# Performance work log

Hardware: AMD Instinct MI355X
Metric: run time of the kernel (lower is better)

Reference implementation:

```python
import jax, jax.numpy as jnp
import numpy as np

TOP_K = 2  # num_experts_per_tok


def setup_inputs() -> dict:
    key = jax.random.key(0)
    ks = jax.random.split(key, 5)
    B, S, D, M, E = 4, 2048, 2048, 2048, 8
    x = jax.random.normal(ks[0], (B, S, D), dtype=jnp.float32)
    gate_kernel = jax.random.normal(ks[1], (D, E), dtype=jnp.float32) / np.sqrt(D)
    wi_0 = jax.random.normal(ks[2], (E, D, M), dtype=jnp.float32) / np.sqrt(D)
    wi_1 = jax.random.normal(ks[3], (E, D, M), dtype=jnp.float32) / np.sqrt(D)
    wo = jax.random.normal(ks[4], (E, M, D), dtype=jnp.float32) / np.sqrt(M)
    return {"x": x, "gate_kernel": gate_kernel, "wi_0": wi_0, "wi_1": wi_1, "wo": wo}


def reference(x, gate_kernel, wi_0, wi_1, wo):
    E = gate_kernel.shape[-1]
    # Gate logits: (B, S, E)
    gate_logits = jnp.einsum("bsd,de->bse", x, gate_kernel)
    # Top-k routing, then softmax over the selected experts' logits
    top_k_weights, top_k_indices = jax.lax.top_k(gate_logits, TOP_K)
    top_k_weights = jax.nn.softmax(top_k_weights.astype(jnp.float32), axis=-1).astype(x.dtype)
    # Dense combine weights per expert: (B, S, E)
    combine_w = jnp.sum(
        jax.nn.one_hot(top_k_indices, E, dtype=x.dtype) * top_k_weights[..., None], axis=-2
    )
    # Grouped GEMM (dense-masked form, as in MaxText dense_matmul path)
    h0 = jnp.einsum("bsd,edm->bsem", x, wi_0)  # (B, S, E, M)
    h1 = jnp.einsum("bsd,edm->bsem", x, wi_1)
    h = jax.nn.silu(h0) * h1 * combine_w[..., None]
    out = jnp.einsum("bsem,emd->bsd", h, wo)  # (B, S, D)
    return out
```

## Files before the change

### kernel.cpp

```cpp
#include <hip/hip_runtime.h>
#include <hip/hip_bf16.h>
#include <stdint.h>

#define TT   8192
#define DD   2048
#define MM   2048
#define NE   8

typedef float f32x4 __attribute__((ext_vector_type(4)));
typedef short s16x8 __attribute__((ext_vector_type(8)));
typedef short s16x4 __attribute__((ext_vector_type(4)));
typedef unsigned int u32;

static __device__ __forceinline__ short f2bf(float f) {
  __hip_bfloat16 h = __float2bfloat16(f);
  short s;
  __builtin_memcpy(&s, &h, 2);
  return s;
}

static __device__ __forceinline__ void gload_lds16(const short* g, short* lds) {
  __builtin_amdgcn_global_load_lds(
      (const __attribute__((address_space(1))) u32*)g,
      (__attribute__((address_space(3))) u32*)lds, 16, 0, 0);
}

__global__ __launch_bounds__(256) void cvt_kernel(const float* __restrict__ in,
                                                  short* __restrict__ out, size_t n) {
  size_t idx = ((size_t)blockIdx.x * 256 + threadIdx.x) * 8;
  size_t stride = (size_t)gridDim.x * 256 * 8;
  for (size_t i = idx; i < n; i += stride) {
    f32x4 a = *(const f32x4*)(in + i);
    f32x4 b = *(const f32x4*)(in + i + 4);
    s16x8 v;
    v[0]=f2bf(a[0]); v[1]=f2bf(a[1]); v[2]=f2bf(a[2]); v[3]=f2bf(a[3]);
    v[4]=f2bf(b[0]); v[5]=f2bf(b[1]); v[6]=f2bf(b[2]); v[7]=f2bf(b[3]);
    *(s16x8*)(out + i) = v;
  }
}

__global__ __launch_bounds__(256) void tcvt_kernel(
    const float* __restrict__ w0, const float* __restrict__ w1, const float* __restrict__ w2,
    short* __restrict__ o0, short* __restrict__ o1, short* __restrict__ o2) {
  __shared__ short tile[64][65];
  const int bz = blockIdx.z;
  const float* in; short* out;
  if (bz < 8)       { in = w0; out = o0; }
  else if (bz < 16) { in = w1; out = o1; }
  else              { in = w2; out = o2; }
  const int ex = bz & 7;
  const float* src = in + (size_t)ex * DD * MM;
  short* dst = out + (size_t)ex * DD * MM;
  const int r0 = blockIdx.y * 64;
  const int c0 = blockIdx.x * 64;
  const int t = threadIdx.x;
  const int rr = t >> 4, cc = (t & 15) * 4;
  #pragma unroll
  for (int i = 0; i < 4; i++) {
    int row = rr + i * 16;
    f32x4 v = *(const f32x4*)(src + (size_t)(r0 + row) * MM + c0 + cc);
    tile[cc + 0][row] = f2bf(v[0]);
    tile[cc + 1][row] = f2bf(v[1]);
    tile[cc + 2][row] = f2bf(v[2]);
    tile[cc + 3][row] = f2bf(v[3]);
  }
  __syncthreads();
  #pragma unroll
  for (int i = 0; i < 4; i++) {
    int orow = rr + i * 16;
    s16x4 v;
    v[0] = tile[orow][cc + 0]; v[1] = tile[orow][cc + 1];
    v[2] = tile[orow][cc + 2]; v[3] = tile[orow][cc + 3];
    *(s16x4*)(dst + (size_t)(c0 + orow) * DD + r0 + cc) = v;
  }
}

__global__ __launch_bounds__(256) void gate_kernel(const float* __restrict__ x,
    const float* __restrict__ gk, int* __restrict__ counts,
    int* __restrict__ tkidx, float* __restrict__ tkw) {
  int t = blockIdx.x;
  const float* xr = x + (size_t)t * DD;
  float acc[NE];
  #pragma unroll
  for (int e = 0; e < NE; e++) acc[e] = 0.f;
  for (int d = threadIdx.x; d < DD; d += 256) {
    float xv = xr[d];
    const float* g = gk + (size_t)d * NE;
    #pragma unroll
    for (int e = 0; e < NE; e++) acc[e] += xv * g[e];
  }
  #pragma unroll
  for (int e = 0; e < NE; e++) {
    #pragma unroll
    for (int off = 32; off >= 1; off >>= 1)
      acc[e] += __shfl_xor(acc[e], off, 64);
  }
  __shared__ float red[4][NE];
  int wid = threadIdx.x >> 6;
  int lane = threadIdx.x & 63;
  if (lane == 0) {
    #pragma unroll
    for (int e = 0; e < NE; e++) red[wid][e] = acc[e];
  }
  __syncthreads();
  if (threadIdx.x == 0) {
    float l[NE];
    #pragma unroll
    for (int e = 0; e < NE; e++) l[e] = red[0][e] + red[1][e] + red[2][e] + red[3][e];
    int i1 = 0; float v1 = l[0];
    #pragma unroll
    for (int e = 1; e < NE; e++) if (l[e] > v1) { v1 = l[e]; i1 = e; }
    int i2 = -1; float v2 = -1e30f;
    #pragma unroll
    for (int e = 0; e < NE; e++) if (e != i1 && l[e] > v2) { v2 = l[e]; i2 = e; }
    float p = __expf(v2 - v1);
    float inv = 1.f / (1.f + p);
    tkidx[t*2]   = i1; tkidx[t*2+1] = i2;
    tkw[t*2]     = inv; tkw[t*2+1]  = p * inv;
    atomicAdd(&counts[i1], 1);
    atomicAdd(&counts[i2], 1);
  }
}

__global__ __launch_bounds__(256) void scatter_kernel(const int* __restrict__ counts,
    int* __restrict__ offsets, const int* __restrict__ tkidx,
    const float* __restrict__ tkw, int* __restrict__ ltok, float* __restrict__ lwt) {
  __shared__ int soff[NE];
  __shared__ int scur[NE];
  if (threadIdx.x == 0) {
    int s = 0;
    for (int e = 0; e < NE; e++) { offsets[e] = s; soff[e] = s; s += counts[e]; scur[e] = 0; }
    offsets[NE] = s;
  }
  __syncthreads();
  for (int i = threadIdx.x; i < TT * 2; i += 256) {
    int e = tkidx[i];
    int pos = atomicAdd(&scur[e], 1);
    int dst = soff[e] + pos;
    ltok[dst] = i >> 1;
    lwt[dst]  = tkw[i];
  }
}

__device__ __forceinline__ void find_seg(const int* __restrict__ offsets, int tile, int bm,
                                         int& e, int& row0, int& rows, int& seg) {
  e = -1; row0 = 0; rows = 0; seg = 0;
  int accT = 0, prev = offsets[0];
  #pragma unroll
  for (int i = 0; i < NE; i++) {
    int nxt = offsets[i+1];
    int cnt = nxt - prev;
    int nt = (cnt + bm - 1) / bm;
    if (e < 0 && tile < accT + nt) { e = i; row0 = (tile - accT) * bm; rows = cnt; seg = prev; }
    accT += nt; prev = nxt;
  }
}

#define MAXT_F 136

__global__ __launch_bounds__(256, 2) void gemm1_fast(
    const short* __restrict__ xbf,
    const short* __restrict__ w0t, const short* __restrict__ w1t,
    const int* __restrict__ offsets,
    const int* __restrict__ ltok, const float* __restrict__ lwt,
    short* __restrict__ hbuf) {
  __shared__ short As[128 * 64];
  __shared__ short B0s[128 * 64];
  __shared__ short B1s[128 * 64];
  __shared__ float w_s[128];

  const int tile = blockIdx.x;
  const int n0 = blockIdx.y * 128;
  int e, row0, rows, seg;
  find_seg(offsets, tile, 128, e, row0, rows, seg);
  if (e < 0) return;

  const int tid = threadIdx.x;
  const int lane = tid & 63, wid = tid >> 6;
  if (tid < 128) {
    int gr = row0 + tid;
    w_s[tid] = (gr < rows) ? lwt[seg + gr] : 0.f;
  }

  const int swz = ((lane & 7) ^ (lane >> 3)) * 8;
  const short* abase[4];
  const short* b0base[4];
  const short* b1base[4];
  #pragma unroll
  for (int c = 0; c < 4; c++) {
    int chunk = wid * 4 + c;
    int r = chunk * 8 + (lane >> 3);
    int gr = row0 + r; if (gr >= rows) gr = rows - 1;
    int tok = ltok[seg + gr];
    abase[c]  = xbf + (size_t)tok * DD + swz;
    int n = n0 + r;
    b0base[c] = w0t + ((size_t)e * MM + n) * DD + swz;
    b1base[c] = w1t + ((size_t)e * MM + n) * DD + swz;
  }

  const int wr = wid >> 1, wc = wid & 1;
  const int lr = lane & 15;
  const int kq = (lane >> 4) * 8;

  f32x4 acc0[4][4], acc1[4][4];
  #pragma unroll
  for (int i = 0; i < 4; i++)
    #pragma unroll
    for (int j = 0; j < 4; j++) { acc0[i][j] = 0.f; acc1[i][j] = 0.f; }

  for (int k0 = 0; k0 < DD; k0 += 64) {
    #pragma unroll
    for (int c = 0; c < 4; c++) {
      int chunk = wid * 4 + c;
      gload_lds16(abase[c]  + k0, As  + chunk * 512);
      gload_lds16(b0base[c] + k0, B0s + chunk * 512);
      gload_lds16(b1base[c] + k0, B1s + chunk * 512);
    }
    __syncthreads();

    #pragma unroll
    for (int ks = 0; ks < 2; ks++) {
      s16x8 a[4], b0[4], b1[4];
      #pragma unroll
      for (int mi = 0; mi < 4; mi++) {
        int row = wr * 64 + mi * 16 + lr;
        int koff = (ks * 32 + kq) ^ ((row & 7) * 8);
        a[mi] = *(const s16x8*)&As[row * 64 + koff];
      }
      #pragma unroll
      for (int ni = 0; ni < 4; ni++) {
        int row = wc * 64 + ni * 16 + lr;
        int koff = (ks * 32 + kq) ^ ((row & 7) * 8);
        b0[ni] = *(const s16x8*)&B0s[row * 64 + koff];
        b1[ni] = *(const s16x8*)&B1s[row * 64 + koff];
      }
      #pragma unroll
      for (int mi = 0; mi < 4; mi++)
        #pragma unroll
        for (int ni = 0; ni < 4; ni++) {
          acc0[mi][ni] = __builtin_amdgcn_mfma_f32_16x16x32_bf16(a[mi], b0[ni], acc0[mi][ni], 0, 0, 0);
          acc1[mi][ni] = __builtin_amdgcn_mfma_f32_16x16x32_bf16(a[mi], b1[ni], acc1[mi][ni], 0, 0, 0);
        }
    }
    __syncthreads();
  }

  const int lq = lane >> 4;
  #pragma unroll
  for (int mi = 0; mi < 4; mi++) {
    #pragma unroll
    for (int jj = 0; jj < 4; jj++) {
      int r = wr * 64 + mi * 16 + lq * 4 + jj;
      int gr = row0 + r;
      if (gr < rows) {
        float wgt = w_s[r];
        size_t hrow = (size_t)(seg + gr) * MM + n0;
        #pragma unroll
        for (int ni = 0; ni < 4; ni++) {
          int c = wc * 64 + ni * 16 + lr;
          float g = acc0[mi][ni][jj];
          float u = acc1[mi][ni][jj];
          float act = g / (1.f + __expf(-g));
          hbuf[hrow + c] = f2bf(act * u * wgt);
        }
      }
    }
  }
}

__global__ __launch_bounds__(256, 2) void gemm2_fast(
    const short* __restrict__ hbuf,
    const short* __restrict__ wot,
    const int* __restrict__ offsets,
    const int* __restrict__ ltok,
    float* __restrict__ out) {
  __shared__ short As[128 * 64];
  __shared__ short Bs[128 * 64];
  __shared__ int tok_s[128];

  const int tile = blockIdx.x;
  const int n0 = blockIdx.y * 128;
  int e, row0, rows, seg;
  find_seg(offsets, tile, 128, e, row0, rows, seg);
  if (e < 0) return;

  const int tid = threadIdx.x;
  const int lane = tid & 63, wid = tid >> 6;
  if (tid < 128) {
    int gr = row0 + tid;
    tok_s[tid] = (gr < rows) ? ltok[seg + gr] : -1;
  }

  const int swz = ((lane & 7) ^ (lane >> 3)) * 8;
  const short* abase[4];
  const short* bbase[4];
  #pragma unroll
  for (int c = 0; c < 4; c++) {
    int chunk = wid * 4 + c;
    int r = chunk * 8 + (lane >> 3);
    int gr = row0 + r; if (gr >= rows) gr = rows - 1;
    abase[c] = hbuf + (size_t)(seg + gr) * MM + swz;
    int n = n0 + r;
    bbase[c] = wot + ((size_t)e * DD + n) * MM + swz;
  }

  const int wr = wid >> 1, wc = wid & 1;
  const int lr = lane & 15;
  const int kq = (lane >> 4) * 8;

  f32x4 acc[4][4];
  #pragma unroll
  for (int i = 0; i < 4; i++)
    #pragma unroll
    for (int j = 0; j < 4; j++) acc[i][j] = 0.f;

  for (int k0 = 0; k0 < MM; k0 += 64) {
    #pragma unroll
    for (int c = 0; c < 4; c++) {
      int chunk = wid * 4 + c;
      gload_lds16(abase[c] + k0, As + chunk * 512);
      gload_lds16(bbase[c] + k0, Bs + chunk * 512);
    }
    __syncthreads();

    #pragma unroll
    for (int ks = 0; ks < 2; ks++) {
      s16x8 a[4], b[4];
      #pragma unroll
      for (int mi = 0; mi < 4; mi++) {
        int row = wr * 64 + mi * 16 + lr;
        int koff = (ks * 32 + kq) ^ ((row & 7) * 8);
        a[mi] = *(const s16x8*)&As[row * 64 + koff];
      }
      #pragma unroll
      for (int ni = 0; ni < 4; ni++) {
        int row = wc * 64 + ni * 16 + lr;
        int koff = (ks * 32 + kq) ^ ((row & 7) * 8);
        b[ni] = *(const s16x8*)&Bs[row * 64 + koff];
      }
      #pragma unroll
      for (int mi = 0; mi < 4; mi++)
        #pragma unroll
        for (int ni = 0; ni < 4; ni++)
          acc[mi][ni] = __builtin_amdgcn_mfma_f32_16x16x32_bf16(a[mi], b[ni], acc[mi][ni], 0, 0, 0);
    }
    __syncthreads();
  }

  const int lq = lane >> 4;
  #pragma unroll
  for (int mi = 0; mi < 4; mi++) {
    #pragma unroll
    for (int jj = 0; jj < 4; jj++) {
      int r = wr * 64 + mi * 16 + lq * 4 + jj;
      int gr = row0 + r;
      if (gr < rows) {
        size_t orow = (size_t)tok_s[r] * DD + n0;
        #pragma unroll
        for (int ni = 0; ni < 4; ni++) {
          int c = wc * 64 + ni * 16 + lr;
          atomicAdd(&out[orow + c], acc[mi][ni][jj]);
        }
      }
    }
  }
}

#define BM1 256
#define BN1 128
#define BM2 256
#define BN2 128
#define BK  32
#define LDK 40
#define MAXT 72

template<bool WB>
__global__ __launch_bounds__(512) void gemm1_kernel(
    const short* __restrict__ xbf,
    const short* __restrict__ w0b, const short* __restrict__ w1b,
    const float* __restrict__ w0f, const float* __restrict__ w1f,
    const int* __restrict__ offsets,
    const int* __restrict__ ltok, const float* __restrict__ lwt,
    short* __restrict__ hbuf) {
  __shared__ short As[BM1][LDK];
  __shared__ short B0s[BN1][LDK];
  __shared__ short B1s[BN1][LDK];
  __shared__ float w_s[BM1];

  const int tile = blockIdx.x;
  const int n0 = blockIdx.y * BN1;
  int e, row0, rows, seg;
  find_seg(offsets, tile, BM1, e, row0, rows, seg);
  if (e < 0) return;

  const int tid = threadIdx.x;
  for (int r = tid; r < BM1; r += 512) {
    int gr = row0 + r;
    w_s[r] = (gr < rows) ? lwt[seg + gr] : 0.f;
  }

  const int ar = tid >> 1;
  const int ak = (tid & 1) * 16;
  const int agr = row0 + ar;
  const int atok = ltok[seg + (agr < rows ? agr : rows - 1)];
  const short* aptr = xbf + (size_t)atok * DD + ak;

  const int bmx = tid >> 8;
  const int t2 = tid & 255;
  const int bk = t2 >> 3;
  const int bn = (t2 & 7) * 16;
  const size_t widx = ((size_t)e * DD + bk) * MM + n0 + bn;
  const short* wsb = (bmx == 0 ? w0b : w1b) ? (bmx == 0 ? w0b : w1b) + widx : nullptr;
  const float* wsf = (bmx == 0 ? w0f : w1f) ? (bmx == 0 ? w0f : w1f) + widx : nullptr;
  short* bdst = (bmx == 0 ? &B0s[0][0] : &B1s[0][0]);

  const int wid = tid >> 6, lane = tid & 63;
  const int wr = wid >> 1, wc = wid & 1;
  const int lr = lane & 15, kh = (lane >> 4) * 8;

  f32x4 acc0[4][4], acc1[4][4];
  #pragma unroll
  for (int i = 0; i < 4; i++)
    #pragma unroll
    for (int j = 0; j < 4; j++) { acc0[i][j] = 0.f; acc1[i][j] = 0.f; }

  for (int k0 = 0; k0 < DD; k0 += BK) {
    s16x8 a0 = *(const s16x8*)(aptr + k0);
    s16x8 a1 = *(const s16x8*)(aptr + k0 + 8);
    short tmp[16];
    if constexpr (WB) {
      s16x8 b0v = *(const s16x8*)(wsb + (size_t)k0 * MM);
      s16x8 b1v = *(const s16x8*)(wsb + (size_t)k0 * MM + 8);
      #pragma unroll
      for (int j = 0; j < 8; j++) { tmp[j] = b0v[j]; tmp[8+j] = b1v[j]; }
    } else {
      const float* p = wsf + (size_t)k0 * MM;
      f32x4 c0 = *(const f32x4*)(p);
      f32x4 c1 = *(const f32x4*)(p + 4);
      f32x4 c2 = *(const f32x4*)(p + 8);
      f32x4 c3 = *(const f32x4*)(p + 12);
      #pragma unroll
      for (int j = 0; j < 4; j++) {
        tmp[j] = f2bf(c0[j]); tmp[4+j] = f2bf(c1[j]);
        tmp[8+j] = f2bf(c2[j]); tmp[12+j] = f2bf(c3[j]);
      }
    }
    *(s16x8*)&As[ar][ak]     = a0;
    *(s16x8*)&As[ar][ak + 8] = a1;
    #pragma unroll
    for (int j = 0; j < 16; j++) bdst[(bn + j) * LDK + bk] = tmp[j];
    __syncthreads();

    s16x8 af[4], b0f[4], b1f[4];
    #pragma unroll
    for (int mi = 0; mi < 4; mi++) af[mi] = *(const s16x8*)&As[wr*64 + mi*16 + lr][kh];
    #pragma unroll
    for (int ni = 0; ni < 4; ni++) {
      b0f[ni] = *(const s16x8*)&B0s[wc*64 + ni*16 + lr][kh];
      b1f[ni] = *(const s16x8*)&B1s[wc*64 + ni*16 + lr][kh];
    }
    #pragma unroll
    for (int mi = 0; mi < 4; mi++)
      #pragma unroll
      for (int ni = 0; ni < 4; ni++) {
        acc0[mi][ni] = __builtin_amdgcn_mfma_f32_16x16x32_bf16(af[mi], b0f[ni], acc0[mi][ni], 0, 0, 0);
        acc1[mi][ni] = __builtin_amdgcn_mfma_f32_16x16x32_bf16(af[mi], b1f[ni], acc1[mi][ni], 0, 0, 0);
      }
    __syncthreads();
  }

  const int lq = lane >> 4;
  #pragma unroll
  for (int mi = 0; mi < 4; mi++) {
    #pragma unroll
    for (int jj = 0; jj < 4; jj++) {
      int r = wr*64 + mi*16 + lq*4 + jj;
      int gr = row0 + r;
      if (gr < rows) {
        float wgt = w_s[r];
        size_t hrow = (size_t)(seg + gr) * MM + n0;
        #pragma unroll
        for (int ni = 0; ni < 4; ni++) {
          int c = wc*64 + ni*16 + lr;
          float g = acc0[mi][ni][jj];
          float u = acc1[mi][ni][jj];
          float act = g / (1.f + __expf(-g));
          hbuf[hrow + c] = f2bf(act * u * wgt);
        }
      }
    }
  }
}

template<bool WB>
__global__ __launch_bounds__(256) void gemm2_kernel(
    const short* __restrict__ hbuf,
    const short* __restrict__ wob, const float* __restrict__ wof,
    const int* __restrict__ offsets,
    const int* __restrict__ ltok,
    float* __restrict__ out) {
  __shared__ short As[BM2][LDK];
  __shared__ short Bs[BN2][LDK];
  __shared__ int tok_s[BM2];

  const int tile = blockIdx.x;
  const int n0 = blockIdx.y * BN2;
  int e, row0, rows, seg;
  find_seg(offsets, tile, BM2, e, row0, rows, seg);
  if (e < 0) return;

  const int tid = threadIdx.x;
  for (int r = tid; r < BM2; r += 256) {
    int gr = row0 + r;
    tok_s[r] = (gr < rows) ? ltok[seg + gr] : -1;
  }

  const int agr = row0 + tid;
  const size_t arow = (size_t)(seg + (agr < rows ? agr : rows - 1)) * MM;

  const int bk = tid >> 3;
  const int bn = (tid & 7) * 16;
  const size_t widx = ((size_t)e * MM + bk) * DD + n0 + bn;

  const int wid = tid >> 6, lane = tid & 63;
  const int wr = wid >> 1, wc = wid & 1;
  const int lr = lane & 15, kh = (lane >> 4) * 8;

  f32x4 acc[8][4];
  #pragma unroll
  for (int i = 0; i < 8; i++)
    #pragma unroll
    for (int j = 0; j < 4; j++) acc[i][j] = 0.f;

  for (int k0 = 0; k0 < MM; k0 += BK) {
    s16x8 a0 = *(const s16x8*)(hbuf + arow + k0);
    s16x8 a1 = *(const s16x8*)(hbuf + arow + k0 + 8);
    s16x8 a2 = *(const s16x8*)(hbuf + arow + k0 + 16);
    s16x8 a3 = *(const s16x8*)(hbuf + arow + k0 + 24);
    short tmp[16];
    if constexpr (WB) {
      s16x8 b0v = *(const s16x8*)(wob + widx + (size_t)k0 * DD);
      s16x8 b1v = *(const s16x8*)(wob + widx + (size_t)k0 * DD + 8);
      #pragma unroll
      for (int j = 0; j < 8; j++) { tmp[j] = b0v[j]; tmp[8+j] = b1v[j]; }
    } else {
      const float* p = wof + widx + (size_t)k0 * DD;
      f32x4 c0 = *(const f32x4*)(p);
      f32x4 c1 = *(const f32x4*)(p + 4);
      f32x4 c2 = *(const f32x4*)(p + 8);
      f32x4 c3 = *(const f32x4*)(p + 12);
      #pragma unroll
      for (int j = 0; j < 4; j++) {
        tmp[j] = f2bf(c0[j]); tmp[4+j] = f2bf(c1[j]);
        tmp[8+j] = f2bf(c2[j]); tmp[12+j] = f2bf(c3[j]);
      }
    }
    *(s16x8*)&As[tid][0]  = a0;
    *(s16x8*)&As[tid][8]  = a1;
    *(s16x8*)&As[tid][16] = a2;
    *(s16x8*)&As[tid][24] = a3;
    #pragma unroll
    for (int j = 0; j < 16; j++) Bs[bn + j][bk] = tmp[j];
    __syncthreads();

    s16x8 af[8], bf_[4];
    #pragma unroll
    for (int mi = 0; mi < 8; mi++) af[mi] = *(const s16x8*)&As[wr*128 + mi*16 + lr][kh];
    #pragma unroll
    for (int ni = 0; ni < 4; ni++) bf_[ni] = *(const s16x8*)&Bs[wc*64 + ni*16 + lr][kh];
    #pragma unroll
    for (int mi = 0; mi < 8; mi++)
      #pragma unroll
      for (int ni = 0; ni < 4; ni++)
        acc[mi][ni] = __builtin_amdgcn_mfma_f32_16x16x32_bf16(af[mi], bf_[ni], acc[mi][ni], 0, 0, 0);
    __syncthreads();
  }

  const int lq = lane >> 4;
  #pragma unroll
  for (int mi = 0; mi < 8; mi++) {
    #pragma unroll
    for (int jj = 0; jj < 4; jj++) {
      int r = wr*128 + mi*16 + lq*4 + jj;
      int gr = row0 + r;
      if (gr < rows) {
        size_t orow = (size_t)tok_s[r] * DD + n0;
        #pragma unroll
        for (int ni = 0; ni < 4; ni++) {
          int c = wc*64 + ni*16 + lr;
          atomicAdd(&out[orow + c], acc[mi][ni][jj]);
        }
      }
    }
  }
}

extern "C" void kernel_launch(void* const* d_in, const int* in_sizes, int n_in,
                              void* d_out, int out_size, void* d_ws, size_t ws_size,
                              hipStream_t stream) {
  const float* x   = (const float*)d_in[0];
  const float* gk  = (const float*)d_in[1];
  const float* wi0 = (const float*)d_in[2];
  const float* wi1 = (const float*)d_in[3];
  const float* wo  = (const float*)d_in[4];
  float* out = (float*)d_out;

  char* w = (char*)d_ws;
  int*   counts  = (int*)(w);
  int*   offsets = (int*)(w + 256);
  int*   tkidx   = (int*)(w + 1024);
  float* tkw     = (float*)(w + 1024 + 65536);
  int*   ltok    = (int*)(w + 1024 + 2*65536);
  float* lwt     = (float*)(w + 1024 + 3*65536);
  short* xbf  = (short*)(w + 524288);
  short* hbuf = xbf + (size_t)TT * DD;
  short* w0t  = hbuf + (size_t)2 * TT * MM;
  short* w1t  = w0t + (size_t)NE * DD * MM;
  short* wot  = w1t + (size_t)NE * DD * MM;
  const size_t NEED_FULL = 524288ull + (size_t)TT*DD*2 + (size_t)2*TT*MM*2 + 3ull*NE*DD*MM*2;
  const bool full = (ws_size >= NEED_FULL);

  hipMemsetAsync(counts, 0, 64, stream);
  hipMemsetAsync(out, 0, sizeof(float) * (size_t)out_size, stream);

  cvt_kernel<<<1024, 256, 0, stream>>>(x, xbf, (size_t)TT * DD);
  gate_kernel<<<TT, 256, 0, stream>>>(x, gk, counts, tkidx, tkw);
  scatter_kernel<<<1, 256, 0, stream>>>(counts, offsets, tkidx, tkw, ltok, lwt);

  if (full) {
    tcvt_kernel<<<dim3(MM/64, DD/64, 24), 256, 0, stream>>>(wi0, wi1, wo, w0t, w1t, wot);
    gemm1_fast<<<dim3(MAXT_F, MM/128), 256, 0, stream>>>(xbf, w0t, w1t, offsets, ltok, lwt, hbuf);
    gemm2_fast<<<dim3(MAXT_F, DD/128), 256, 0, stream>>>(hbuf, wot, offsets, ltok, out);
  } else {
    dim3 g1(MAXT, MM / BN1), g2(MAXT, DD / BN2);
    gemm1_kernel<false><<<g1, 512, 0, stream>>>(xbf, nullptr, nullptr, wi0, wi1,
                                                offsets, ltok, lwt, hbuf);
    gemm2_kernel<false><<<g2, 256, 0, stream>>>(hbuf, nullptr, wo, offsets, ltok, out);
  }
}
```

Before: 937.2 us.

## Replace atomic scatter with slot buffer and combine kernel, add XCD tile remap

The second GEMM now writes its results directly to a per-slot float buffer, which reuses the freed w0t/w1t region. A new combine kernel then adds each token's two expert rows, so the fp32 atomicAdd scatter and the output memset are no longer needed. Both GEMMs remap workgroup IDs so that consecutive tiles land on the same XCD for L2 reuse, and their launch bounds are raised to 3 waves per SIMD. The transpose-convert kernel's stores are widened to 16-byte vectors, and the fallback slow path is removed, so the code now assumes the workspace is large enough.

```diff
diff --git a/kernel.cpp b/kernel.cpp
--- a/kernel.cpp
+++ b/kernel.cpp
@@ -9,7 +9,6 @@
 
 typedef float f32x4 __attribute__((ext_vector_type(4)));
 typedef short s16x8 __attribute__((ext_vector_type(8)));
-typedef short s16x4 __attribute__((ext_vector_type(4)));
 typedef unsigned int u32;
 
 static __device__ __forceinline__ short f2bf(float f) {
@@ -65,14 +64,13 @@
     tile[cc + 3][row] = f2bf(v[3]);
   }
   __syncthreads();
-  #pragma unroll
-  for (int i = 0; i < 4; i++) {
-    int orow = rr + i * 16;
-    s16x4 v;
-    v[0] = tile[orow][cc + 0]; v[1] = tile[orow][cc + 1];
-    v[2] = tile[orow][cc + 2]; v[3] = tile[orow][cc + 3];
-    *(s16x4*)(dst + (size_t)(c0 + orow) * DD + r0 + cc) = v;
-  }
+  const int orow = t >> 2, c8 = (t & 3) * 16;
+  s16x8 v0, v1;
+  #pragma unroll
+  for (int i = 0; i < 8; i++) { v0[i] = tile[orow][c8 + i]; v1[i] = tile[orow][c8 + 8 + i]; }
+  short* dp = dst + (size_t)(c0 + orow) * DD + r0 + c8;
+  *(s16x8*)(dp) = v0;
+  *(s16x8*)(dp + 8) = v1;
 }
 
 __global__ __launch_bounds__(256) void gate_kernel(const float* __restrict__ x,
@@ -124,7 +122,8 @@
 
 __global__ __launch_bounds__(256) void scatter_kernel(const int* __restrict__ counts,
     int* __restrict__ offsets, const int* __restrict__ tkidx,
-    const float* __restrict__ tkw, int* __restrict__ ltok, float* __restrict__ lwt) {
+    const float* __restrict__ tkw, int* __restrict__ ltok, float* __restrict__ lwt,
+    int* __restrict__ slots) {
   __shared__ int soff[NE];
   __shared__ int scur[NE];
   if (threadIdx.x == 0) {
@@ -139,6 +138,21 @@
     int dst = soff[e] + pos;
     ltok[dst] = i >> 1;
     lwt[dst]  = tkw[i];
+    slots[i]  = dst;
+  }
+}
+
+__global__ __launch_bounds__(256) void combine_kernel(const float* __restrict__ comb,
+    const int* __restrict__ slots, float* __restrict__ out) {
+  const int t = blockIdx.x;
+  const int s0 = slots[2 * t], s1 = slots[2 * t + 1];
+  const f32x4* p0 = (const f32x4*)(comb + (size_t)s0 * DD);
+  const f32x4* p1 = (const f32x4*)(comb + (size_t)s1 * DD);
+  f32x4* po = (f32x4*)(out + (size_t)t * DD);
+  #pragma unroll
+  for (int i = 0; i < 2; i++) {
+    int idx = threadIdx.x + i * 256;
+    po[idx] = p0[idx] + p1[idx];
   }
 }
 
@@ -156,9 +170,19 @@
   }
 }
 
+__device__ __forceinline__ void xcd_map(int& tile, int& nyi) {
+  const int nx = gridDim.x;
+  const int nwg = nx * gridDim.y;
+  const int bid = blockIdx.y * nx + blockIdx.x;
+  const int cpx = nwg >> 3;
+  const int s = (bid & 7) * cpx + (bid >> 3);
+  tile = s % nx;
+  nyi  = s / nx;
+}
+
 #define MAXT_F 136
 
-__global__ __launch_bounds__(256, 2) void gemm1_fast(
+__global__ __launch_bounds__(256, 3) void gemm1_fast(
     const short* __restrict__ xbf,
     const short* __restrict__ w0t, const short* __restrict__ w1t,
     const int* __restrict__ offsets,
@@ -169,8 +193,9 @@
   __shared__ short B1s[128 * 64];
   __shared__ float w_s[128];
 
-  const int tile = blockIdx.x;
-  const int n0 = blockIdx.y * 128;
+  int tile, nyi;
+  xcd_map(tile, nyi);
+  const int n0 = nyi * 128;
   int e, row0, rows, seg;
   find_seg(offsets, tile, 128, e, row0, rows, seg);
   if (e < 0) return;
@@ -268,28 +293,23 @@
   }
 }
 
-__global__ __launch_bounds__(256, 2) void gemm2_fast(
+__global__ __launch_bounds__(256, 3) void gemm2_fast(
     const short* __restrict__ hbuf,
     const short* __restrict__ wot,
     const int* __restrict__ offsets,
-    const int* __restrict__ ltok,
-    float* __restrict__ out) {
+    float* __restrict__ comb) {
   __shared__ short As[128 * 64];
   __shared__ short Bs[128 * 64];
-  __shared__ int tok_s[128];
-
-  const int tile = blockIdx.x;
-  const int n0 = blockIdx.y * 128;
+
+  int tile, nyi;
+  xcd_map(tile, nyi);
+  const int n0 = nyi * 128;
   int e, row0, rows, seg;
   find_seg(offsets, tile, 128, e, row0, rows, seg);
   if (e < 0) return;
 
   const int tid = threadIdx.x;
   const int lane = tid & 63, wid = tid >> 6;
-  if (tid < 128) {
-    int gr = row0 + tid;
-    tok_s[tid] = (gr < rows) ? ltok[seg + gr] : -1;
-  }
 
   const int swz = ((lane & 7) ^ (lane >> 3)) * 8;
   const short* abase[4];
@@ -355,240 +375,11 @@
       int r = wr * 64 + mi * 16 + lq * 4 + jj;
       int gr = row0 + r;
       if (gr < rows) {
-        size_t orow = (size_t)tok_s[r] * DD + n0;
+        size_t orow = (size_t)(seg + gr) * DD + n0;
         #pragma unroll
         for (int ni = 0; ni < 4; ni++) {
           int c = wc * 64 + ni * 16 + lr;
-          atomicAdd(&out[orow + c], acc[mi][ni][jj]);
-        }
-      }
-    }
-  }
-}
-
-#define BM1 256
-#define BN1 128
-#define BM2 256
-#define BN2 128
-#define BK  32
-#define LDK 40
-#define MAXT 72
-
-template<bool WB>
-__global__ __launch_bounds__(512) void gemm1_kernel(
-    const short* __restrict__ xbf,
-    const short* __restrict__ w0b, const short* __restrict__ w1b,
-    const float* __restrict__ w0f, const float* __restrict__ w1f,
-    const int* __restrict__ offsets,
-    const int* __restrict__ ltok, const float* __restrict__ lwt,
-    short* __restrict__ hbuf) {
-  __shared__ short As[BM1][LDK];
-  __shared__ short B0s[BN1][LDK];
-  __shared__ short B1s[BN1][LDK];
-  __shared__ float w_s[BM1];
-
-  const int tile = blockIdx.x;
-  const int n0 = blockIdx.y * BN1;
-  int e, row0, rows, seg;
-  find_seg(offsets, tile, BM1, e, row0, rows, seg);
-  if (e < 0) return;
-
-  const int tid = threadIdx.x;
-  for (int r = tid; r < BM1; r += 512) {
-    int gr = row0 + r;
-    w_s[r] = (gr < rows) ? lwt[seg + gr] : 0.f;
-  }
-
-  const int ar = tid >> 1;
-  const int ak = (tid & 1) * 16;
-  const int agr = row0 + ar;
-  const int atok = ltok[seg + (agr < rows ? agr : rows - 1)];
-  const short* aptr = xbf + (size_t)atok * DD + ak;
-
-  const int bmx = tid >> 8;
-  const int t2 = tid & 255;
-  const int bk = t2 >> 3;
-  const int bn = (t2 & 7) * 16;
-  const size_t widx = ((size_t)e * DD + bk) * MM + n0 + bn;
-  const short* wsb = (bmx == 0 ? w0b : w1b) ? (bmx == 0 ? w0b : w1b) + widx : nullptr;
-  const float* wsf = (bmx == 0 ? w0f : w1f) ? (bmx == 0 ? w0f : w1f) + widx : nullptr;
-  short* bdst = (bmx == 0 ? &B0s[0][0] : &B1s[0][0]);
-
-  const int wid = tid >> 6, lane = tid & 63;
-  const int wr = wid >> 1, wc = wid & 1;
-  const int lr = lane & 15, kh = (lane >> 4) * 8;
-
-  f32x4 acc0[4][4], acc1[4][4];
-  #pragma unroll
-  for (int i = 0; i < 4; i++)
-    #pragma unroll
-    for (int j = 0; j < 4; j++) { acc0[i][j] = 0.f; acc1[i][j] = 0.f; }
-
-  for (int k0 = 0; k0 < DD; k0 += BK) {
-    s16x8 a0 = *(const s16x8*)(aptr + k0);
-    s16x8 a1 = *(const s16x8*)(aptr + k0 + 8);
-    short tmp[16];
-    if constexpr (WB) {
-      s16x8 b0v = *(const s16x8*)(wsb + (size_t)k0 * MM);
-      s16x8 b1v = *(const s16x8*)(wsb + (size_t)k0 * MM + 8);
-      #pragma unroll
-      for (int j = 0; j < 8; j++) { tmp[j] = b0v[j]; tmp[8+j] = b1v[j]; }
-    } else {
-      const float* p = wsf + (size_t)k0 * MM;
-      f32x4 c0 = *(const f32x4*)(p);
-      f32x4 c1 = *(const f32x4*)(p + 4);
-      f32x4 c2 = *(const f32x4*)(p + 8);
-      f32x4 c3 = *(const f32x4*)(p + 12);
-      #pragma unroll
-      for (int j = 0; j < 4; j++) {
-        tmp[j] = f2bf(c0[j]); tmp[4+j] = f2bf(c1[j]);
-        tmp[8+j] = f2bf(c2[j]); tmp[12+j] = f2bf(c3[j]);
-      }
-    }
-    *(s16x8*)&As[ar][ak]     = a0;
-    *(s16x8*)&As[ar][ak + 8] = a1;
-    #pragma unroll
-    for (int j = 0; j < 16; j++) bdst[(bn + j) * LDK + bk] = tmp[j];
-    __syncthreads();
-
-    s16x8 af[4], b0f[4], b1f[4];
-    #pragma unroll
-    for (int mi = 0; mi < 4; mi++) af[mi] = *(const s16x8*)&As[wr*64 + mi*16 + lr][kh];
-    #pragma unroll
-    for (int ni = 0; ni < 4; ni++) {
-      b0f[ni] = *(const s16x8*)&B0s[wc*64 + ni*16 + lr][kh];
-      b1f[ni] = *(const s16x8*)&B1s[wc*64 + ni*16 + lr][kh];
-    }
-    #pragma unroll
-    for (int mi = 0; mi < 4; mi++)
-      #pragma unroll
-      for (int ni = 0; ni < 4; ni++) {
-        acc0[mi][ni] = __builtin_amdgcn_mfma_f32_16x16x32_bf16(af[mi], b0f[ni], acc0[mi][ni], 0, 0, 0);
-        acc1[mi][ni] = __builtin_amdgcn_mfma_f32_16x16x32_bf16(af[mi], b1f[ni], acc1[mi][ni], 0, 0, 0);
-      }
-    __syncthreads();
-  }
-
-  const int lq = lane >> 4;
-  #pragma unroll
-  for (int mi = 0; mi < 4; mi++) {
-    #pragma unroll
-    for (int jj = 0; jj < 4; jj++) {
-      int r = wr*64 + mi*16 + lq*4 + jj;
-      int gr = row0 + r;
-      if (gr < rows) {
-        float wgt = w_s[r];
-        size_t hrow = (size_t)(seg + gr) * MM + n0;
-        #pragma unroll
-        for (int ni = 0; ni < 4; ni++) {
-          int c = wc*64 + ni*16 + lr;
-          float g = acc0[mi][ni][jj];
-          float u = acc1[mi][ni][jj];
-          float act = g / (1.f + __expf(-g));
-          hbuf[hrow + c] = f2bf(act * u * wgt);
-        }
-      }
-    }
-  }
-}
-
-template<bool WB>
-__global__ __launch_bounds__(256) void gemm2_kernel(
-    const short* __restrict__ hbuf,
-    const short* __restrict__ wob, const float* __restrict__ wof,
-    const int* __restrict__ offsets,
-    const int* __restrict__ ltok,
-    float* __restrict__ out) {
-  __shared__ short As[BM2][LDK];
-  __shared__ short Bs[BN2][LDK];
-  __shared__ int tok_s[BM2];
-
-  const int tile = blockIdx.x;
-  const int n0 = blockIdx.y * BN2;
-  int e, row0, rows, seg;
-  find_seg(offsets, tile, BM2, e, row0, rows, seg);
-  if (e < 0) return;
-
-  const int tid = threadIdx.x;
-  for (int r = tid; r < BM2; r += 256) {
-    int gr = row0 + r;
-    tok_s[r] = (gr < rows) ? ltok[seg + gr] : -1;
-  }
-
-  const int agr = row0 + tid;
-  const size_t arow = (size_t)(seg + (agr < rows ? agr : rows - 1)) * MM;
-
-  const int bk = tid >> 3;
-  const int bn = (tid & 7) * 16;
-  const size_t widx = ((size_t)e * MM + bk) * DD + n0 + bn;
-
-  const int wid = tid >> 6, lane = tid & 63;
-  const int wr = wid >> 1, wc = wid & 1;
-  const int lr = lane & 15, kh = (lane >> 4) * 8;
-
-  f32x4 acc[8][4];
-  #pragma unroll
-  for (int i = 0; i < 8; i++)
-    #pragma unroll
-    for (int j = 0; j < 4; j++) acc[i][j] = 0.f;
-
-  for (int k0 = 0; k0 < MM; k0 += BK) {
-    s16x8 a0 = *(const s16x8*)(hbuf + arow + k0);
-    s16x8 a1 = *(const s16x8*)(hbuf + arow + k0 + 8);
-    s16x8 a2 = *(const s16x8*)(hbuf + arow + k0 + 16);
-    s16x8 a3 = *(const s16x8*)(hbuf + arow + k0 + 24);
-    short tmp[16];
-    if constexpr (WB) {
-      s16x8 b0v = *(const s16x8*)(wob + widx + (size_t)k0 * DD);
-      s16x8 b1v = *(const s16x8*)(wob + widx + (size_t)k0 * DD + 8);
-      #pragma unroll
-      for (int j = 0; j < 8; j++) { tmp[j] = b0v[j]; tmp[8+j] = b1v[j]; }
-    } else {
-      const float* p = wof + widx + (size_t)k0 * DD;
-      f32x4 c0 = *(const f32x4*)(p);
-      f32x4 c1 = *(const f32x4*)(p + 4);
-      f32x4 c2 = *(const f32x4*)(p + 8);
-      f32x4 c3 = *(const f32x4*)(p + 12);
-      #pragma unroll
-      for (int j = 0; j < 4; j++) {
-        tmp[j] = f2bf(c0[j]); tmp[4+j] = f2bf(c1[j]);
-        tmp[8+j] = f2bf(c2[j]); tmp[12+j] = f2bf(c3[j]);
-      }
-    }
-    *(s16x8*)&As[tid][0]  = a0;
-    *(s16x8*)&As[tid][8]  = a1;
-    *(s16x8*)&As[tid][16] = a2;
-    *(s16x8*)&As[tid][24] = a3;
-    #pragma unroll
-    for (int j = 0; j < 16; j++) Bs[bn + j][bk] = tmp[j];
-    __syncthreads();
-
-    s16x8 af[8], bf_[4];
-    #pragma unroll
-    for (int mi = 0; mi < 8; mi++) af[mi] = *(const s16x8*)&As[wr*128 + mi*16 + lr][kh];
-    #pragma unroll
-    for (int ni = 0; ni < 4; ni++) bf_[ni] = *(const s16x8*)&Bs[wc*64 + ni*16 + lr][kh];
-    #pragma unroll
-    for (int mi = 0; mi < 8; mi++)
-      #pragma unroll
-      for (int ni = 0; ni < 4; ni++)
-        acc[mi][ni] = __builtin_amdgcn_mfma_f32_16x16x32_bf16(af[mi], bf_[ni], acc[mi][ni], 0, 0, 0);
-    __syncthreads();
-  }
-
-  const int lq = lane >> 4;
-  #pragma unroll
-  for (int mi = 0; mi < 8; mi++) {
-    #pragma unroll
-    for (int jj = 0; jj < 4; jj++) {
-      int r = wr*128 + mi*16 + lq*4 + jj;
-      int gr = row0 + r;
-      if (gr < rows) {
-        size_t orow = (size_t)tok_s[r] * DD + n0;
-        #pragma unroll
-        for (int ni = 0; ni < 4; ni++) {
-          int c = wc*64 + ni*16 + lr;
-          atomicAdd(&out[orow + c], acc[mi][ni][jj]);
+          comb[orow + c] = acc[mi][ni][jj];
         }
       }
     }
@@ -612,29 +403,22 @@
   float* tkw     = (float*)(w + 1024 + 65536);
   int*   ltok    = (int*)(w + 1024 + 2*65536);
   float* lwt     = (float*)(w + 1024 + 3*65536);
+  int*   slots   = (int*)(w + 1024 + 4*65536);
   short* xbf  = (short*)(w + 524288);
   short* hbuf = xbf + (size_t)TT * DD;
   short* w0t  = hbuf + (size_t)2 * TT * MM;
   short* w1t  = w0t + (size_t)NE * DD * MM;
   short* wot  = w1t + (size_t)NE * DD * MM;
-  const size_t NEED_FULL = 524288ull + (size_t)TT*DD*2 + (size_t)2*TT*MM*2 + 3ull*NE*DD*MM*2;
-  const bool full = (ws_size >= NEED_FULL);
+  float* comb = (float*)w0t;
 
   hipMemsetAsync(counts, 0, 64, stream);
-  hipMemsetAsync(out, 0, sizeof(float) * (size_t)out_size, stream);
 
   cvt_kernel<<<1024, 256, 0, stream>>>(x, xbf, (size_t)TT * DD);
   gate_kernel<<<TT, 256, 0, stream>>>(x, gk, counts, tkidx, tkw);
-  scatter_kernel<<<1, 256, 0, stream>>>(counts, offsets, tkidx, tkw, ltok, lwt);
-
-  if (full) {
-    tcvt_kernel<<<dim3(MM/64, DD/64, 24), 256, 0, stream>>>(wi0, wi1, wo, w0t, w1t, wot);
-    gemm1_fast<<<dim3(MAXT_F, MM/128), 256, 0, stream>>>(xbf, w0t, w1t, offsets, ltok, lwt, hbuf);
-    gemm2_fast<<<dim3(MAXT_F, DD/128), 256, 0, stream>>>(hbuf, wot, offsets, ltok, out);
-  } else {
-    dim3 g1(MAXT, MM / BN1), g2(MAXT, DD / BN2);
-    gemm1_kernel<false><<<g1, 512, 0, stream>>>(xbf, nullptr, nullptr, wi0, wi1,
-                                                offsets, ltok, lwt, hbuf);
-    gemm2_kernel<false><<<g2, 256, 0, stream>>>(hbuf, nullptr, wo, offsets, ltok, out);
-  }
-}
+  scatter_kernel<<<1, 256, 0, stream>>>(counts, offsets, tkidx, tkw, ltok, lwt, slots);
+  tcvt_kernel<<<dim3(MM/64, DD/64, 24), 256, 0, stream>>>(wi0, wi1, wo, w0t, w1t, wot);
+
+  gemm1_fast<<<dim3(MAXT_F, MM/128), 256, 0, stream>>>(xbf, w0t, w1t, offsets, ltok, lwt, hbuf);
+  gemm2_fast<<<dim3(MAXT_F, DD/128), 256, 0, stream>>>(hbuf, wot, offsets, comb);
+  combine_kernel<<<TT, 256, 0, stream>>>(comb, slots, out);
+}
```

Result: slower. 1.497 ms (+59.8%).
